# Kernel tuning notes

Hardware: AMD Instinct MI355X
Metric: run time of the kernel (lower is better)

The kernel has to match this reference:

```python
import jax, jax.numpy as jnp
import numpy as np

# ---- module config (from init_kwargs) ----
KERNEL_SIZE = 3
DIM = 3
HALF = KERNEL_SIZE // 2          # kernel offsets span [-HALF, HALF]
COORD_RANGE = 256                # voxel grid extent per spatial axis
NUM_BATCH = 4
N_VOXELS = 100_000
FEAT_DIM = 32
STRIDE = COORD_RANGE + 2 * HALF  # encoding stride so shifted coords fit


def _kernel_offsets():
    # All offsets of a KERNEL_SIZE^DIM kernel, centered (MinkowskiEngine-style).
    r = np.arange(-HALF, HALF + 1)
    grids = np.meshgrid(*([r] * DIM), indexing='ij')
    return jnp.asarray(np.stack([g.ravel() for g in grids], axis=1), dtype=jnp.int32)  # [K, DIM]


def setup_inputs() -> dict:
    key = jax.random.key(0)
    k1, k2, k3 = jax.random.split(key, 3)
    batch = jax.random.randint(k1, (1, N_VOXELS), 0, NUM_BATCH, dtype=jnp.int32)
    coords = jax.random.randint(k2, (3, N_VOXELS), 0, COORD_RANGE, dtype=jnp.int32)
    sparse_indices = jnp.concatenate([batch, coords], axis=0)  # [4, N]
    features = jax.random.normal(k3, (N_VOXELS, FEAT_DIM), dtype=jnp.float32)
    return {"sparse_indices": sparse_indices, "features": features}


def _kernel_map_and_out_key(sparse_indices):
    offsets = _kernel_offsets()                 # [K, 3]
    K = offsets.shape[0]
    b = sparse_indices[0].astype(jnp.int32)     # [N]
    coords = sparse_indices[1:].T.astype(jnp.int32)  # [N, 3]
    N = coords.shape[0]
    NK = N * K

    # neighbor coords per (voxel, offset); shift by HALF so values are >= 0
    nbr = coords[:, None, :] + offsets[None, :, :] + HALF     # [N, K, 3]
    S = STRIDE
    # unique integer hash of (batch, x, y, z); fits in int32 for these ranges
    enc = ((b[:, None] * S + nbr[..., 0]) * S + nbr[..., 1]) * S + nbr[..., 2]
    enc = enc.reshape(-1)                                     # [NK]

    # unique keys (sorted) + inverse map; pad to static size NK
    uniq, inv = jnp.unique(enc, return_inverse=True, size=NK, fill_value=-1)

    # reorder unique keys into first-seen order to match the dict-based reference
    first = jnp.full((NK,), NK, dtype=jnp.int32).at[inv].min(
        jnp.arange(NK, dtype=jnp.int32))
    order = jnp.argsort(first)                                # padding sorts last
    new_id = jnp.zeros((NK,), dtype=jnp.int32).at[order].set(
        jnp.arange(NK, dtype=jnp.int32))
    out_idx = new_id[inv]                                     # [NK] output index per entry

    # decode unique (first-seen ordered) keys back to spatial coords
    uo = uniq[order]
    valid = uo >= 0
    z = uo % S
    y = (uo // S) % S
    x = (uo // (S * S)) % S
    out_key = jnp.stack([x, y, z], axis=1) - HALF             # undo shift
    out_key = jnp.where(valid[:, None], out_key, -1)          # [NK, 3], padded rows = -1

    input_idx = jnp.repeat(jnp.arange(N, dtype=jnp.int32), K) # [NK]
    rel_pos = jnp.tile(jnp.arange(K, dtype=jnp.int32), N)     # [NK]
    kernel_map = jnp.stack([input_idx, out_idx, rel_pos], axis=1)  # [NK, 3]
    return kernel_map, out_key


def reference(sparse_indices, features):
    kernel_map, out_key = _kernel_map_and_out_key(sparse_indices)
    NK = kernel_map.shape[0]
    # canonical downstream use of the kernel map: gather inputs, scatter-sum to outputs
    out_feats = jax.ops.segment_sum(features[kernel_map[:, 0]],
                                    kernel_map[:, 1], num_segments=NK)
    return kernel_map, out_key, out_feats
```

## Files before the change

### kernel.cpp

```cpp
#include <hip/hip_runtime.h>
#include <stdint.h>

typedef unsigned long long u64;
typedef unsigned u32;
typedef float __attribute__((ext_vector_type(4))) f4raw;

#define K 27
#define S 258
#define ENCMAX (4 * S * S * S)

__global__ void k_mark(const int* __restrict__ si, int N,
                       u64* __restrict__ bits, u64* __restrict__ dupb) {
    int idx = blockIdx.x * blockDim.x + threadIdx.x;
    if (idx >= N * 9) return;
    int n = idx / 9, run = idx - n * 9;
    int ox = run / 3, oy = run - ox * 3;
    int b = si[n], x = si[N + n], y = si[2 * N + n], z = si[3 * N + n];
    unsigned enc0 = (unsigned)(((b * S + x + ox) * S + (y + oy)) * S + z);
    unsigned w = enc0 >> 6; int bit = enc0 & 63;
    u64 m1 = 7ull << bit;
    u64 old = atomicOr(&bits[w], m1);
    u64 d1 = old & m1;
    if (d1) atomicOr(&dupb[w], d1);
    if (bit > 61) {
        u64 m2 = 7ull >> (64 - bit);
        u64 old2 = atomicOr(&bits[w + 1], m2);
        u64 d2 = old2 & m2;
        if (d2) atomicOr(&dupb[w + 1], d2);
    }
}

__global__ void s1_tilesum(const u64* __restrict__ bits, int* __restrict__ tsums) {
    __shared__ int s[256];
    int tid = threadIdx.x;
    const u64* p = bits + (size_t)blockIdx.x * 4096;
    int sum = 0;
    for (int j = tid; j < 4096; j += 256) sum += __popcll(p[j]);
    s[tid] = sum; __syncthreads();
    for (int off = 128; off > 0; off >>= 1) {
        if (tid < off) s[tid] += s[tid + off];
        __syncthreads();
    }
    if (tid == 0) tsums[blockIdx.x] = s[0];
}

__global__ void s3_wprefix(const u64* __restrict__ bits, const int* __restrict__ tsums,
                           u32* __restrict__ wprefix) {
    __shared__ int s[256];
    __shared__ int tbase;
    int tid = threadIdx.x;
    int pre = 0;
    for (int j = tid; j < (int)blockIdx.x; j += 256) pre += tsums[j];
    s[tid] = pre; __syncthreads();
    for (int off = 128; off > 0; off >>= 1) {
        if (tid < off) s[tid] += s[tid + off];
        __syncthreads();
    }
    if (tid == 0) tbase = s[0];
    __syncthreads();
    size_t base = (size_t)blockIdx.x * 4096 + (size_t)tid * 16;
    int pc[16]; int tsum = 0;
#pragma unroll
    for (int j = 0; j < 16; j++) { pc[j] = __popcll(bits[base + j]); tsum += pc[j]; }
    s[tid] = tsum; __syncthreads();
    for (int off = 1; off < 256; off <<= 1) {
        int t = (tid >= off) ? s[tid - off] : 0;
        __syncthreads();
        s[tid] += t;
        __syncthreads();
    }
    int run = tbase + s[tid] - tsum;
#pragma unroll
    for (int j = 0; j < 16; j++) { wprefix[base + j] = (u32)run; run += pc[j]; }
}

__global__ void k_kid(const int* __restrict__ si, int N,
                      const u64* __restrict__ bits, const u64* __restrict__ dupb,
                      const u32* __restrict__ wprefix,
                      int* __restrict__ kid, int* __restrict__ minE) {
    int idx = blockIdx.x * blockDim.x + threadIdx.x;
    if (idx >= N * 9) return;
    int n = idx / 9, run = idx - n * 9;
    int ox = run / 3, oy = run - ox * 3;
    int b = si[n], x = si[N + n], y = si[2 * N + n], z = si[3 * N + n];
    unsigned enc0 = (unsigned)(((b * S + x + ox) * S + (y + oy)) * S + z);
    int e0 = n * K + run * 3;
#pragma unroll
    for (int oz = 0; oz < 3; ++oz) {
        unsigned enc = enc0 + oz;
        unsigned w = enc >> 6; int bit = enc & 63;
        int kd = (int)wprefix[w] + __popcll(bits[w] & ((1ull << bit) - 1));
        int multi = (int)((dupb[w] >> bit) & 1);
        kid[e0 + oz] = multi ? (int)((u32)kd | 0x80000000u) : kd;
        if (multi) atomicMin(&minE[kd], e0 + oz);
    }
}

__global__ void k_flagsum(const int* __restrict__ kid, const int* __restrict__ minE,
                          int NK, int* __restrict__ bsums) {
    __shared__ int s[256];
    int tid = threadIdx.x;
    int base = blockIdx.x * 4096 + tid * 16;
    int kv[16];
    *(int4*)(kv + 0)  = *(const int4*)(kid + base + 0);
    *(int4*)(kv + 4)  = *(const int4*)(kid + base + 4);
    *(int4*)(kv + 8)  = *(const int4*)(kid + base + 8);
    *(int4*)(kv + 12) = *(const int4*)(kid + base + 12);
    int sum = 0;
#pragma unroll
    for (int j = 0; j < 16; j++) {
        int e = base + j;
        if (e < NK) {
            int v = kv[j];
            sum += (v >= 0) ? 1 : (minE[v & 0x7FFFFFFF] == e ? 1 : 0);
        }
    }
    s[tid] = sum; __syncthreads();
    for (int off = 128; off > 0; off >>= 1) {
        if (tid < off) s[tid] += s[tid + off];
        __syncthreads();
    }
    if (tid == 0) bsums[blockIdx.x] = s[0];
}

__global__ void k_scanC(int* __restrict__ kid, const int* __restrict__ minE,
                        const int* __restrict__ bsums, const int* __restrict__ si,
                        int N, int NK, int NB,
                        float* __restrict__ out_key, int* __restrict__ rank_key,
                        float4* __restrict__ outF4) {
    __shared__ int s[256];
    __shared__ u64 s2[256];
    int tid = threadIdx.x;
    u64 acc = 0;
    for (int j = tid; j < NB; j += 256) {
        u64 b = (u64)(u32)bsums[j];
        acc += b << 32;
        if (j < (int)blockIdx.x) acc += b;
    }
    s2[tid] = acc; __syncthreads();
    for (int off = 128; off > 0; off >>= 1) {
        if (tid < off) s2[tid] += s2[tid + off];
        __syncthreads();
    }
    int blockoff = (int)(u32)(s2[0] & 0xFFFFFFFFull);
    int U = (int)(s2[0] >> 32);

    int base = blockIdx.x * 4096 + tid * 16;
    int kv[16];
    *(int4*)(kv + 0)  = *(const int4*)(kid + base + 0);
    *(int4*)(kv + 4)  = *(const int4*)(kid + base + 4);
    *(int4*)(kv + 8)  = *(const int4*)(kid + base + 8);
    *(int4*)(kv + 12) = *(const int4*)(kid + base + 12);
    int fbits = 0;
#pragma unroll
    for (int j = 0; j < 16; j++) {
        int e = base + j;
        int f = 0;
        if (e < NK) {
            int v = kv[j];
            f = (v >= 0) ? 1 : (minE[v & 0x7FFFFFFF] == e ? 1 : 0);
        }
        fbits |= f << j;
    }
    int tsum = __popc(fbits);
    s[tid] = tsum; __syncthreads();
    for (int off = 1; off < 256; off <<= 1) {
        int t = (tid >= off) ? s[tid - off] : 0;
        __syncthreads();
        s[tid] += t;
        __syncthreads();
    }
    int offset = blockoff + s[tid] - tsum;
    float4 zf = {0.f, 0.f, 0.f, 0.f};
    int run = 0;
#pragma unroll
    for (int j = 0; j < 16; j++) {
        int e = base + j;
        if ((fbits >> j) & 1) {
            int rank = offset + run;
            int n = e / K; int m = e - n * K;
            int x = si[N + n], y = si[2 * N + n], z = si[3 * N + n];
            int ox = m / 9; int rm = m - ox * 9; int oy = rm / 3; int oz = rm - oy * 3;
            out_key[(size_t)rank * 3 + 0] = (float)(x + ox - 1);
            out_key[(size_t)rank * 3 + 1] = (float)(y + oy - 1);
            out_key[(size_t)rank * 3 + 2] = (float)(z + oz - 1);
            int v = kv[j];
            if (v < 0) {
                int kd = v & 0x7FFFFFFF;
                rank_key[kd] = rank;
                kid[e] = rank | 0x40000000;
                float4* q = outF4 + (size_t)rank * 8;
#pragma unroll
                for (int q8 = 0; q8 < 8; q8++) q[q8] = zf;
            } else {
                kid[e] = rank;
            }
            run++;
        }
    }
    int rows = NK - U;
    int gs = gridDim.x * blockDim.x;
    for (int i = blockIdx.x * blockDim.x + tid; i < rows; i += gs) {
        int row = U + i;
        float4* q = outF4 + (size_t)row * 8;
#pragma unroll
        for (int q8 = 0; q8 < 8; q8++) q[q8] = zf;
        out_key[(size_t)row * 3 + 0] = -1.0f;
        out_key[(size_t)row * 3 + 1] = -1.0f;
        out_key[(size_t)row * 3 + 2] = -1.0f;
    }
}

__global__ void k_final(const int* __restrict__ ent, const int* __restrict__ rank_key,
                        const float4* __restrict__ feat4,
                        float* __restrict__ km, float* __restrict__ outF, int NK) {
    int total = NK * 8;
    int gs = gridDim.x * blockDim.x;
    for (int idx = blockIdx.x * blockDim.x + threadIdx.x; idx < total; idx += gs) {
        int e = idx >> 3, g = idx & 7;
        int v = ent[e];
        int n = e / K, m = e - n * K;
        float4 val = feat4[(size_t)n * 8 + g];
        int uid, atom;
        if (v < 0)                { uid = rank_key[v & 0x7FFFFFFF]; atom = 1; }
        else if (v & 0x40000000)  { uid = v & 0x3FFFFFFF;           atom = 1; }
        else                      { uid = v;                        atom = 0; }
        float* dst = outF + (size_t)uid * 32 + g * 4;
        if (atom) {
            atomicAdd(dst + 0, val.x);
            atomicAdd(dst + 1, val.y);
            atomicAdd(dst + 2, val.z);
            atomicAdd(dst + 3, val.w);
        } else {
            f4raw vr = {val.x, val.y, val.z, val.w};
            __builtin_nontemporal_store(vr, (f4raw*)dst);
        }
        if (g < 3)
            km[(size_t)e * 3 + g] = (g == 0) ? (float)n
                                   : ((g == 1) ? (float)uid : (float)m);
    }
}

extern "C" void kernel_launch(void* const* d_in, const int* in_sizes, int n_in,
                              void* d_out, int out_size, void* d_ws, size_t ws_size,
                              hipStream_t stream) {
    const int* si = (const int*)d_in[0];
    const float4* feat4 = (const float4*)d_in[1];
    int N = in_sizes[0] / 4;
    int NK = N * K;
    int NKp = (NK + 4095) & ~4095;
    int NB = NKp / 4096;

    int NW = (ENCMAX + 63) / 64;
    int NT = (NW + 4095) / 4096;
    int NWp = NT * 4096;

    float* km = (float*)d_out;
    float* out_key = km + (size_t)NK * 3;
    float* outF = km + (size_t)NK * 6;

    char* w = (char*)d_ws;
    char* p_bits  = w; w += ((size_t)NWp * 8 + 15) & ~(size_t)15;
    char* p_dupb  = w; w += ((size_t)NWp * 8 + 15) & ~(size_t)15;
    size_t zbytes = (size_t)(w - (char*)d_ws);
    char* p_tsums = w; w += ((size_t)(NT + 1) * 4 + 15) & ~(size_t)15;
    char* p_wpref = w; w += ((size_t)NWp * 4 + 15) & ~(size_t)15;
    char* p_minE  = w; w += ((size_t)NK * 4 + 15) & ~(size_t)15;
    char* p_kid   = w; w += ((size_t)NKp * 4 + 15) & ~(size_t)15;
    char* p_rank  = w; w += ((size_t)NK * 4 + 15) & ~(size_t)15;
    char* p_bsums = w; w += ((size_t)(NB + 1) * 4 + 15) & ~(size_t)15;

    u64* bits     = (u64*)p_bits;
    u64* dupb     = (u64*)p_dupb;
    int* tsums    = (int*)p_tsums;
    u32* wprefix  = (u32*)p_wpref;
    int* minE     = (int*)p_minE;
    int* kid      = (int*)p_kid;
    int* rank_key = (int*)p_rank;
    int* bsums    = (int*)p_bsums;

    (void)hipMemsetAsync(d_ws, 0, zbytes, stream);
    (void)hipMemsetAsync(minE, 0x7F, (size_t)NK * 4, stream);

    int nb9 = (N * 9 + 255) / 256;
    k_mark<<<nb9, 256, 0, stream>>>(si, N, bits, dupb);
    s1_tilesum<<<NT, 256, 0, stream>>>(bits, tsums);
    s3_wprefix<<<NT, 256, 0, stream>>>(bits, tsums, wprefix);
    k_kid<<<nb9, 256, 0, stream>>>(si, N, bits, dupb, wprefix, kid, minE);
    k_flagsum<<<NB, 256, 0, stream>>>(kid, minE, NK, bsums);
    k_scanC<<<NB, 256, 0, stream>>>(kid, minE, bsums, si, N, NK, NB,
                                    out_key, rank_key, (float4*)outF);
    k_final<<<2048, 256, 0, stream>>>(kid, rank_key, feat4, km, outF, NK);
}
```

Measured before the change: 607.8 us.

## Fuse hashing and scan stages into one persistent kernel with grid barriers

Merges the mark, tile-sum, word-prefix, kid, flag-sum and scan kernels into a single kernel launched with NB blocks. Hand-written atomic-counter grid barriers separate the phases. Per-entry kid values stay in registers between the kid and scan phases instead of being written and re-read, which removes several kernel launches and one global round trip. This relies on all NB blocks being resident at once (launch_bounds 256,3); if they are not, the barriers deadlock. The kid phase now works in contiguous per-thread entry chunks, so it recomputes the encoding for each entry.

```diff
diff --git a/kernel.cpp b/kernel.cpp
--- a/kernel.cpp
+++ b/kernel.cpp
@@ -9,148 +9,110 @@
 #define S 258
 #define ENCMAX (4 * S * S * S)
 
-__global__ void k_mark(const int* __restrict__ si, int N,
-                       u64* __restrict__ bits, u64* __restrict__ dupb) {
-    int idx = blockIdx.x * blockDim.x + threadIdx.x;
-    if (idx >= N * 9) return;
-    int n = idx / 9, run = idx - n * 9;
-    int ox = run / 3, oy = run - ox * 3;
-    int b = si[n], x = si[N + n], y = si[2 * N + n], z = si[3 * N + n];
-    unsigned enc0 = (unsigned)(((b * S + x + ox) * S + (y + oy)) * S + z);
-    unsigned w = enc0 >> 6; int bit = enc0 & 63;
-    u64 m1 = 7ull << bit;
-    u64 old = atomicOr(&bits[w], m1);
-    u64 d1 = old & m1;
-    if (d1) atomicOr(&dupb[w], d1);
-    if (bit > 61) {
-        u64 m2 = 7ull >> (64 - bit);
-        u64 old2 = atomicOr(&bits[w + 1], m2);
-        u64 d2 = old2 & m2;
-        if (d2) atomicOr(&dupb[w + 1], d2);
-    }
-}
-
-__global__ void s1_tilesum(const u64* __restrict__ bits, int* __restrict__ tsums) {
+__device__ __forceinline__ void gbar(int* cnt, int nblk) {
+    __syncthreads();
+    if (threadIdx.x == 0) {
+        __threadfence();
+        __hip_atomic_fetch_add(cnt, 1, __ATOMIC_RELEASE, __HIP_MEMORY_SCOPE_AGENT);
+        while (__hip_atomic_load(cnt, __ATOMIC_RELAXED, __HIP_MEMORY_SCOPE_AGENT) < nblk)
+            __builtin_amdgcn_s_sleep(2);
+        (void)__hip_atomic_load(cnt, __ATOMIC_ACQUIRE, __HIP_MEMORY_SCOPE_AGENT);
+        __threadfence();
+    }
+    __syncthreads();
+}
+
+__global__ void __launch_bounds__(256, 3)
+k_fused(const int* __restrict__ si, int N, int NK, int NT, int NB,
+        u64* __restrict__ bits, u64* __restrict__ dupb,
+        int* __restrict__ tsums, u32* __restrict__ wprefix,
+        int* __restrict__ minE, int* __restrict__ kid,
+        int* __restrict__ rank_key, float* __restrict__ out_key,
+        float4* __restrict__ outF4, int* __restrict__ barcnt) {
     __shared__ int s[256];
-    int tid = threadIdx.x;
-    const u64* p = bits + (size_t)blockIdx.x * 4096;
-    int sum = 0;
-    for (int j = tid; j < 4096; j += 256) sum += __popcll(p[j]);
-    s[tid] = sum; __syncthreads();
-    for (int off = 128; off > 0; off >>= 1) {
-        if (tid < off) s[tid] += s[tid + off];
-        __syncthreads();
-    }
-    if (tid == 0) tsums[blockIdx.x] = s[0];
-}
-
-__global__ void s3_wprefix(const u64* __restrict__ bits, const int* __restrict__ tsums,
-                           u32* __restrict__ wprefix) {
-    __shared__ int s[256];
-    __shared__ int tbase;
-    int tid = threadIdx.x;
-    int pre = 0;
-    for (int j = tid; j < (int)blockIdx.x; j += 256) pre += tsums[j];
-    s[tid] = pre; __syncthreads();
-    for (int off = 128; off > 0; off >>= 1) {
-        if (tid < off) s[tid] += s[tid + off];
-        __syncthreads();
-    }
-    if (tid == 0) tbase = s[0];
-    __syncthreads();
-    size_t base = (size_t)blockIdx.x * 4096 + (size_t)tid * 16;
+    __shared__ u64 s2[256];
+    const int tid = threadIdx.x;
+    const int b = blockIdx.x;
+    const int nblk = gridDim.x;
+    const int gs = nblk * 256;
+
+    for (int idx = b * 256 + tid; idx < N * 9; idx += gs) {
+        int n = idx / 9, run = idx - n * 9;
+        int ox = run / 3, oy = run - ox * 3;
+        int bb = si[n], x = si[N + n], y = si[2 * N + n], z = si[3 * N + n];
+        unsigned enc0 = (unsigned)(((bb * S + x + ox) * S + (y + oy)) * S + z);
+        unsigned w = enc0 >> 6; int bit = enc0 & 63;
+        u64 m1 = 7ull << bit;
+        u64 old = atomicOr(&bits[w], m1);
+        u64 d1 = old & m1;
+        if (d1) atomicOr(&dupb[w], d1);
+        if (bit > 61) {
+            u64 m2 = 7ull >> (64 - bit);
+            u64 old2 = atomicOr(&bits[w + 1], m2);
+            u64 d2 = old2 & m2;
+            if (d2) atomicOr(&dupb[w + 1], d2);
+        }
+    }
+    gbar(barcnt + 0, nblk);
+
     int pc[16]; int tsum = 0;
-#pragma unroll
-    for (int j = 0; j < 16; j++) { pc[j] = __popcll(bits[base + j]); tsum += pc[j]; }
-    s[tid] = tsum; __syncthreads();
-    for (int off = 1; off < 256; off <<= 1) {
-        int t = (tid >= off) ? s[tid - off] : 0;
-        __syncthreads();
-        s[tid] += t;
-        __syncthreads();
-    }
-    int run = tbase + s[tid] - tsum;
-#pragma unroll
-    for (int j = 0; j < 16; j++) { wprefix[base + j] = (u32)run; run += pc[j]; }
-}
-
-__global__ void k_kid(const int* __restrict__ si, int N,
-                      const u64* __restrict__ bits, const u64* __restrict__ dupb,
-                      const u32* __restrict__ wprefix,
-                      int* __restrict__ kid, int* __restrict__ minE) {
-    int idx = blockIdx.x * blockDim.x + threadIdx.x;
-    if (idx >= N * 9) return;
-    int n = idx / 9, run = idx - n * 9;
-    int ox = run / 3, oy = run - ox * 3;
-    int b = si[n], x = si[N + n], y = si[2 * N + n], z = si[3 * N + n];
-    unsigned enc0 = (unsigned)(((b * S + x + ox) * S + (y + oy)) * S + z);
-    int e0 = n * K + run * 3;
-#pragma unroll
-    for (int oz = 0; oz < 3; ++oz) {
-        unsigned enc = enc0 + oz;
-        unsigned w = enc >> 6; int bit = enc & 63;
-        int kd = (int)wprefix[w] + __popcll(bits[w] & ((1ull << bit) - 1));
-        int multi = (int)((dupb[w] >> bit) & 1);
-        kid[e0 + oz] = multi ? (int)((u32)kd | 0x80000000u) : kd;
-        if (multi) atomicMin(&minE[kd], e0 + oz);
-    }
-}
-
-__global__ void k_flagsum(const int* __restrict__ kid, const int* __restrict__ minE,
-                          int NK, int* __restrict__ bsums) {
-    __shared__ int s[256];
-    int tid = threadIdx.x;
-    int base = blockIdx.x * 4096 + tid * 16;
+    if (b < NT) {
+        size_t wb = (size_t)b * 4096 + (size_t)tid * 16;
+#pragma unroll
+        for (int j = 0; j < 16; j++) { pc[j] = __popcll(bits[wb + j]); tsum += pc[j]; }
+        s[tid] = tsum; __syncthreads();
+        for (int off = 128; off > 0; off >>= 1) {
+            if (tid < off) s[tid] += s[tid + off];
+            __syncthreads();
+        }
+        if (tid == 0) tsums[b] = s[0];
+    }
+    gbar(barcnt + 1, nblk);
+
+    if (b < NT) {
+        int pre = 0;
+        for (int j = tid; j < b; j += 256) pre += tsums[j];
+        s[tid] = pre; __syncthreads();
+        for (int off = 128; off > 0; off >>= 1) {
+            if (tid < off) s[tid] += s[tid + off];
+            __syncthreads();
+        }
+        int tbase = s[0];
+        __syncthreads();
+        s[tid] = tsum; __syncthreads();
+        for (int off = 1; off < 256; off <<= 1) {
+            int t = (tid >= off) ? s[tid - off] : 0;
+            __syncthreads();
+            s[tid] += t;
+            __syncthreads();
+        }
+        int run = tbase + s[tid] - tsum;
+        size_t wb = (size_t)b * 4096 + (size_t)tid * 16;
+#pragma unroll
+        for (int j = 0; j < 16; j++) { wprefix[wb + j] = (u32)run; run += pc[j]; }
+    }
+    gbar(barcnt + 2, nblk);
+
+    const int base = b * 4096 + tid * 16;
     int kv[16];
-    *(int4*)(kv + 0)  = *(const int4*)(kid + base + 0);
-    *(int4*)(kv + 4)  = *(const int4*)(kid + base + 4);
-    *(int4*)(kv + 8)  = *(const int4*)(kid + base + 8);
-    *(int4*)(kv + 12) = *(const int4*)(kid + base + 12);
-    int sum = 0;
 #pragma unroll
     for (int j = 0; j < 16; j++) {
         int e = base + j;
+        kv[j] = 0;
         if (e < NK) {
-            int v = kv[j];
-            sum += (v >= 0) ? 1 : (minE[v & 0x7FFFFFFF] == e ? 1 : 0);
-        }
-    }
-    s[tid] = sum; __syncthreads();
-    for (int off = 128; off > 0; off >>= 1) {
-        if (tid < off) s[tid] += s[tid + off];
-        __syncthreads();
-    }
-    if (tid == 0) bsums[blockIdx.x] = s[0];
-}
-
-__global__ void k_scanC(int* __restrict__ kid, const int* __restrict__ minE,
-                        const int* __restrict__ bsums, const int* __restrict__ si,
-                        int N, int NK, int NB,
-                        float* __restrict__ out_key, int* __restrict__ rank_key,
-                        float4* __restrict__ outF4) {
-    __shared__ int s[256];
-    __shared__ u64 s2[256];
-    int tid = threadIdx.x;
-    u64 acc = 0;
-    for (int j = tid; j < NB; j += 256) {
-        u64 b = (u64)(u32)bsums[j];
-        acc += b << 32;
-        if (j < (int)blockIdx.x) acc += b;
-    }
-    s2[tid] = acc; __syncthreads();
-    for (int off = 128; off > 0; off >>= 1) {
-        if (tid < off) s2[tid] += s2[tid + off];
-        __syncthreads();
-    }
-    int blockoff = (int)(u32)(s2[0] & 0xFFFFFFFFull);
-    int U = (int)(s2[0] >> 32);
-
-    int base = blockIdx.x * 4096 + tid * 16;
-    int kv[16];
-    *(int4*)(kv + 0)  = *(const int4*)(kid + base + 0);
-    *(int4*)(kv + 4)  = *(const int4*)(kid + base + 4);
-    *(int4*)(kv + 8)  = *(const int4*)(kid + base + 8);
-    *(int4*)(kv + 12) = *(const int4*)(kid + base + 12);
+            int n = e / K; int m = e - n * K;
+            int ox = m / 9; int rm = m - ox * 9; int oy = rm / 3; int oz = rm - oy * 3;
+            int bb = si[n], x = si[N + n], y = si[2 * N + n], z = si[3 * N + n];
+            unsigned enc = (unsigned)(((bb * S + x + ox) * S + (y + oy)) * S + (z + oz));
+            unsigned w = enc >> 6; int bit = enc & 63;
+            int kd = (int)wprefix[w] + __popcll(bits[w] & ((1ull << bit) - 1));
+            int multi = (int)((dupb[w] >> bit) & 1);
+            kv[j] = multi ? (int)((u32)kd | 0x80000000u) : kd;
+            if (multi) atomicMin(&minE[kd], e);
+        }
+    }
+    gbar(barcnt + 3, nblk);
+
     int fbits = 0;
 #pragma unroll
     for (int j = 0; j < 16; j++) {
@@ -162,45 +124,71 @@
         }
         fbits |= f << j;
     }
-    int tsum = __popc(fbits);
-    s[tid] = tsum; __syncthreads();
+    int fsum = __popc(fbits);
+    s[tid] = fsum; __syncthreads();
+    for (int off = 128; off > 0; off >>= 1) {
+        if (tid < off) s[tid] += s[tid + off];
+        __syncthreads();
+    }
+    if (tid == 0) tsums[NT + 1 + b] = s[0];
+    gbar(barcnt + 4, nblk);
+
+    const int* bsums = tsums + NT + 1;
+    u64 acc = 0;
+    for (int j = tid; j < NB; j += 256) {
+        u64 v = (u64)(u32)bsums[j];
+        acc += v << 32;
+        if (j < b) acc += v;
+    }
+    s2[tid] = acc; __syncthreads();
+    for (int off = 128; off > 0; off >>= 1) {
+        if (tid < off) s2[tid] += s2[tid + off];
+        __syncthreads();
+    }
+    int blockoff = (int)(u32)(s2[0] & 0xFFFFFFFFull);
+    int U = (int)(s2[0] >> 32);
+    __syncthreads();
+    s[tid] = fsum; __syncthreads();
     for (int off = 1; off < 256; off <<= 1) {
         int t = (tid >= off) ? s[tid - off] : 0;
         __syncthreads();
         s[tid] += t;
         __syncthreads();
     }
-    int offset = blockoff + s[tid] - tsum;
+    int offset = blockoff + s[tid] - fsum;
     float4 zf = {0.f, 0.f, 0.f, 0.f};
     int run = 0;
 #pragma unroll
     for (int j = 0; j < 16; j++) {
         int e = base + j;
-        if ((fbits >> j) & 1) {
-            int rank = offset + run;
-            int n = e / K; int m = e - n * K;
-            int x = si[N + n], y = si[2 * N + n], z = si[3 * N + n];
-            int ox = m / 9; int rm = m - ox * 9; int oy = rm / 3; int oz = rm - oy * 3;
-            out_key[(size_t)rank * 3 + 0] = (float)(x + ox - 1);
-            out_key[(size_t)rank * 3 + 1] = (float)(y + oy - 1);
-            out_key[(size_t)rank * 3 + 2] = (float)(z + oz - 1);
+        if (e < NK) {
             int v = kv[j];
-            if (v < 0) {
-                int kd = v & 0x7FFFFFFF;
-                rank_key[kd] = rank;
-                kid[e] = rank | 0x40000000;
-                float4* q = outF4 + (size_t)rank * 8;
-#pragma unroll
-                for (int q8 = 0; q8 < 8; q8++) q[q8] = zf;
+            if ((fbits >> j) & 1) {
+                int rank = offset + run;
+                int n = e / K; int m = e - n * K;
+                int x = si[N + n], y = si[2 * N + n], z = si[3 * N + n];
+                int ox = m / 9; int rm = m - ox * 9; int oy = rm / 3; int oz = rm - oy * 3;
+                out_key[(size_t)rank * 3 + 0] = (float)(x + ox - 1);
+                out_key[(size_t)rank * 3 + 1] = (float)(y + oy - 1);
+                out_key[(size_t)rank * 3 + 2] = (float)(z + oz - 1);
+                if (v < 0) {
+                    int kd = v & 0x7FFFFFFF;
+                    rank_key[kd] = rank;
+                    kid[e] = rank | 0x40000000;
+                    float4* q = outF4 + (size_t)rank * 8;
+#pragma unroll
+                    for (int q8 = 0; q8 < 8; q8++) q[q8] = zf;
+                } else {
+                    kid[e] = rank;
+                }
+                run++;
             } else {
-                kid[e] = rank;
+                kid[e] = v;
             }
-            run++;
         }
     }
     int rows = NK - U;
-    int gs = gridDim.x * blockDim.x;
-    for (int i = blockIdx.x * blockDim.x + tid; i < rows; i += gs) {
+    for (int i = b * 256 + tid; i < rows; i += gs) {
         int row = U + i;
         float4* q = outF4 + (size_t)row * 8;
 #pragma unroll
@@ -260,16 +248,17 @@
     float* outF = km + (size_t)NK * 6;
 
     char* w = (char*)d_ws;
+    char* p_bar   = w; w += 64;
     char* p_bits  = w; w += ((size_t)NWp * 8 + 15) & ~(size_t)15;
     char* p_dupb  = w; w += ((size_t)NWp * 8 + 15) & ~(size_t)15;
     size_t zbytes = (size_t)(w - (char*)d_ws);
-    char* p_tsums = w; w += ((size_t)(NT + 1) * 4 + 15) & ~(size_t)15;
+    char* p_tsums = w; w += ((size_t)(NT + 1 + NB + 1) * 4 + 15) & ~(size_t)15;
     char* p_wpref = w; w += ((size_t)NWp * 4 + 15) & ~(size_t)15;
     char* p_minE  = w; w += ((size_t)NK * 4 + 15) & ~(size_t)15;
     char* p_kid   = w; w += ((size_t)NKp * 4 + 15) & ~(size_t)15;
     char* p_rank  = w; w += ((size_t)NK * 4 + 15) & ~(size_t)15;
-    char* p_bsums = w; w += ((size_t)(NB + 1) * 4 + 15) & ~(size_t)15;
-
+
+    int* barcnt   = (int*)p_bar;
     u64* bits     = (u64*)p_bits;
     u64* dupb     = (u64*)p_dupb;
     int* tsums    = (int*)p_tsums;
@@ -277,18 +266,12 @@
     int* minE     = (int*)p_minE;
     int* kid      = (int*)p_kid;
     int* rank_key = (int*)p_rank;
-    int* bsums    = (int*)p_bsums;
 
     (void)hipMemsetAsync(d_ws, 0, zbytes, stream);
     (void)hipMemsetAsync(minE, 0x7F, (size_t)NK * 4, stream);
 
-    int nb9 = (N * 9 + 255) / 256;
-    k_mark<<<nb9, 256, 0, stream>>>(si, N, bits, dupb);
-    s1_tilesum<<<NT, 256, 0, stream>>>(bits, tsums);
-    s3_wprefix<<<NT, 256, 0, stream>>>(bits, tsums, wprefix);
-    k_kid<<<nb9, 256, 0, stream>>>(si, N, bits, dupb, wprefix, kid, minE);
-    k_flagsum<<<NB, 256, 0, stream>>>(kid, minE, NK, bsums);
-    k_scanC<<<NB, 256, 0, stream>>>(kid, minE, bsums, si, N, NK, NB,
-                                    out_key, rank_key, (float4*)outF);
+    k_fused<<<NB, 256, 0, stream>>>(si, N, NK, NT, NB, bits, dupb, tsums, wprefix,
+                                    minE, kid, rank_key, out_key, (float4*)outF,
+                                    barcnt);
     k_final<<<2048, 256, 0, stream>>>(kid, rank_key, feat4, km, outF, NK);
 }
```

Result: slower. 1.114 ms (+83.2%).

## Interleave occupancy bits, dup flag and word prefix into 16-byte records

Applied to the files above, without the earlier changes.

Packs the occupancy bitmap word, a per-word duplicate flag and the per-word prefix count into a single 16-byte record. This lets k_kid fetch everything for a lookup with one vector load instead of three scattered loads. Duplicate tracking becomes a coarse per-word flag, so more entries may take the atomic path. The bitmap scans in s1_tilesum and s3_wprefix now read with a stride of two. k_final also switches from a grid-stride loop to one thread per element.

```diff
diff --git a/kernel.cpp b/kernel.cpp
--- a/kernel.cpp
+++ b/kernel.cpp
@@ -9,8 +9,8 @@
 #define S 258
 #define ENCMAX (4 * S * S * S)
 
-__global__ void k_mark(const int* __restrict__ si, int N,
-                       u64* __restrict__ bits, u64* __restrict__ dupb) {
+
+__global__ void k_mark(const int* __restrict__ si, int N, u64* __restrict__ rec) {
     int idx = blockIdx.x * blockDim.x + threadIdx.x;
     if (idx >= N * 9) return;
     int n = idx / 9, run = idx - n * 9;
@@ -19,23 +19,21 @@
     unsigned enc0 = (unsigned)(((b * S + x + ox) * S + (y + oy)) * S + z);
     unsigned w = enc0 >> 6; int bit = enc0 & 63;
     u64 m1 = 7ull << bit;
-    u64 old = atomicOr(&bits[w], m1);
-    u64 d1 = old & m1;
-    if (d1) atomicOr(&dupb[w], d1);
+    u64 old = atomicOr(&rec[2 * (size_t)w], m1);
+    if (old & m1) atomicOr((u32*)rec + 4 * (size_t)w + 2, 1u);
     if (bit > 61) {
         u64 m2 = 7ull >> (64 - bit);
-        u64 old2 = atomicOr(&bits[w + 1], m2);
-        u64 d2 = old2 & m2;
-        if (d2) atomicOr(&dupb[w + 1], d2);
-    }
-}
-
-__global__ void s1_tilesum(const u64* __restrict__ bits, int* __restrict__ tsums) {
+        u64 old2 = atomicOr(&rec[2 * (size_t)(w + 1)], m2);
+        if (old2 & m2) atomicOr((u32*)rec + 4 * (size_t)(w + 1) + 2, 1u);
+    }
+}
+
+__global__ void s1_tilesum(const u64* __restrict__ rec, int* __restrict__ tsums) {
     __shared__ int s[256];
     int tid = threadIdx.x;
-    const u64* p = bits + (size_t)blockIdx.x * 4096;
+    const u64* p = rec + (size_t)blockIdx.x * 8192;
     int sum = 0;
-    for (int j = tid; j < 4096; j += 256) sum += __popcll(p[j]);
+    for (int j = tid; j < 4096; j += 256) sum += __popcll(p[2 * j]);
     s[tid] = sum; __syncthreads();
     for (int off = 128; off > 0; off >>= 1) {
         if (tid < off) s[tid] += s[tid + off];
@@ -44,10 +42,10 @@
     if (tid == 0) tsums[blockIdx.x] = s[0];
 }
 
-__global__ void s3_wprefix(const u64* __restrict__ bits, const int* __restrict__ tsums,
-                           u32* __restrict__ wprefix) {
+__global__ void s3_wprefix(u64* __restrict__ rec, const int* __restrict__ tsums,
+                           int NT) {
     __shared__ int s[256];
-    __shared__ int tbase;
+    __shared__ int tb;
     int tid = threadIdx.x;
     int pre = 0;
     for (int j = tid; j < (int)blockIdx.x; j += 256) pre += tsums[j];
@@ -56,12 +54,13 @@
         if (tid < off) s[tid] += s[tid + off];
         __syncthreads();
     }
-    if (tid == 0) tbase = s[0];
+    if (tid == 0) tb = s[0];
     __syncthreads();
-    size_t base = (size_t)blockIdx.x * 4096 + (size_t)tid * 16;
+    int tbase = tb;
+    size_t wb = (size_t)blockIdx.x * 4096 + (size_t)tid * 16;
     int pc[16]; int tsum = 0;
 #pragma unroll
-    for (int j = 0; j < 16; j++) { pc[j] = __popcll(bits[base + j]); tsum += pc[j]; }
+    for (int j = 0; j < 16; j++) { pc[j] = __popcll(rec[2 * (wb + j)]); tsum += pc[j]; }
     s[tid] = tsum; __syncthreads();
     for (int off = 1; off < 256; off <<= 1) {
         int t = (tid >= off) ? s[tid - off] : 0;
@@ -70,13 +69,13 @@
         __syncthreads();
     }
     int run = tbase + s[tid] - tsum;
-#pragma unroll
-    for (int j = 0; j < 16; j++) { wprefix[base + j] = (u32)run; run += pc[j]; }
+    u32* rec32 = (u32*)rec;
+#pragma unroll
+    for (int j = 0; j < 16; j++) { rec32[4 * (wb + j) + 3] = (u32)run; run += pc[j]; }
 }
 
 __global__ void k_kid(const int* __restrict__ si, int N,
-                      const u64* __restrict__ bits, const u64* __restrict__ dupb,
-                      const u32* __restrict__ wprefix,
+                      const u64* __restrict__ rec,
                       int* __restrict__ kid, int* __restrict__ minE) {
     int idx = blockIdx.x * blockDim.x + threadIdx.x;
     if (idx >= N * 9) return;
@@ -84,13 +83,25 @@
     int ox = run / 3, oy = run - ox * 3;
     int b = si[n], x = si[N + n], y = si[2 * N + n], z = si[3 * N + n];
     unsigned enc0 = (unsigned)(((b * S + x + ox) * S + (y + oy)) * S + z);
+    unsigned w = enc0 >> 6; int bit = enc0 & 63;
+    ulonglong2 r0 = *(const ulonglong2*)(rec + 2 * (size_t)w);
+    u64 bb0 = r0.x; u32 du0 = (u32)r0.y; u32 wp0 = (u32)(r0.y >> 32);
+    u64 bb1 = 0; u32 du1 = 0, wp1 = 0;
+    if (bit > 61) {
+        ulonglong2 r1 = *(const ulonglong2*)(rec + 2 * (size_t)(w + 1));
+        bb1 = r1.x; du1 = (u32)r1.y; wp1 = (u32)(r1.y >> 32);
+    }
     int e0 = n * K + run * 3;
 #pragma unroll
     for (int oz = 0; oz < 3; ++oz) {
         unsigned enc = enc0 + oz;
-        unsigned w = enc >> 6; int bit = enc & 63;
-        int kd = (int)wprefix[w] + __popcll(bits[w] & ((1ull << bit) - 1));
-        int multi = (int)((dupb[w] >> bit) & 1);
+        int bit2 = enc & 63;
+        bool hi = (enc >> 6) != w;
+        u64 bbw = hi ? bb1 : bb0;
+        u32 wp  = hi ? wp1 : wp0;
+        u32 du  = hi ? du1 : du0;
+        int kd = (int)wp + __popcll(bbw & ((1ull << bit2) - 1));
+        int multi = (du != 0);
         kid[e0 + oz] = multi ? (int)((u32)kd | 0x80000000u) : kd;
         if (multi) atomicMin(&minE[kd], e0 + oz);
     }
@@ -214,31 +225,29 @@
 __global__ void k_final(const int* __restrict__ ent, const int* __restrict__ rank_key,
                         const float4* __restrict__ feat4,
                         float* __restrict__ km, float* __restrict__ outF, int NK) {
-    int total = NK * 8;
-    int gs = gridDim.x * blockDim.x;
-    for (int idx = blockIdx.x * blockDim.x + threadIdx.x; idx < total; idx += gs) {
-        int e = idx >> 3, g = idx & 7;
-        int v = ent[e];
-        int n = e / K, m = e - n * K;
-        float4 val = feat4[(size_t)n * 8 + g];
-        int uid, atom;
-        if (v < 0)                { uid = rank_key[v & 0x7FFFFFFF]; atom = 1; }
-        else if (v & 0x40000000)  { uid = v & 0x3FFFFFFF;           atom = 1; }
-        else                      { uid = v;                        atom = 0; }
-        float* dst = outF + (size_t)uid * 32 + g * 4;
-        if (atom) {
-            atomicAdd(dst + 0, val.x);
-            atomicAdd(dst + 1, val.y);
-            atomicAdd(dst + 2, val.z);
-            atomicAdd(dst + 3, val.w);
-        } else {
-            f4raw vr = {val.x, val.y, val.z, val.w};
-            __builtin_nontemporal_store(vr, (f4raw*)dst);
-        }
-        if (g < 3)
-            km[(size_t)e * 3 + g] = (g == 0) ? (float)n
-                                   : ((g == 1) ? (float)uid : (float)m);
-    }
+    int idx = blockIdx.x * blockDim.x + threadIdx.x;
+    if (idx >= NK * 8) return;
+    int e = idx >> 3, g = idx & 7;
+    int v = ent[e];
+    int n = e / K, m = e - n * K;
+    float4 val = feat4[(size_t)n * 8 + g];
+    int uid, atom;
+    if (v < 0)                { uid = rank_key[v & 0x7FFFFFFF]; atom = 1; }
+    else if (v & 0x40000000)  { uid = v & 0x3FFFFFFF;           atom = 1; }
+    else                      { uid = v;                        atom = 0; }
+    float* dst = outF + (size_t)uid * 32 + g * 4;
+    if (atom) {
+        atomicAdd(dst + 0, val.x);
+        atomicAdd(dst + 1, val.y);
+        atomicAdd(dst + 2, val.z);
+        atomicAdd(dst + 3, val.w);
+    } else {
+        f4raw vr = {val.x, val.y, val.z, val.w};
+        __builtin_nontemporal_store(vr, (f4raw*)dst);
+    }
+    if (g < 3)
+        km[(size_t)e * 3 + g] = (g == 0) ? (float)n
+                               : ((g == 1) ? (float)uid : (float)m);
 }
 
 extern "C" void kernel_launch(void* const* d_in, const int* in_sizes, int n_in,
@@ -260,20 +269,16 @@
     float* outF = km + (size_t)NK * 6;
 
     char* w = (char*)d_ws;
-    char* p_bits  = w; w += ((size_t)NWp * 8 + 15) & ~(size_t)15;
-    char* p_dupb  = w; w += ((size_t)NWp * 8 + 15) & ~(size_t)15;
+    char* p_rec   = w; w += ((size_t)NWp * 16 + 15) & ~(size_t)15;
     size_t zbytes = (size_t)(w - (char*)d_ws);
     char* p_tsums = w; w += ((size_t)(NT + 1) * 4 + 15) & ~(size_t)15;
-    char* p_wpref = w; w += ((size_t)NWp * 4 + 15) & ~(size_t)15;
     char* p_minE  = w; w += ((size_t)NK * 4 + 15) & ~(size_t)15;
     char* p_kid   = w; w += ((size_t)NKp * 4 + 15) & ~(size_t)15;
     char* p_rank  = w; w += ((size_t)NK * 4 + 15) & ~(size_t)15;
     char* p_bsums = w; w += ((size_t)(NB + 1) * 4 + 15) & ~(size_t)15;
 
-    u64* bits     = (u64*)p_bits;
-    u64* dupb     = (u64*)p_dupb;
+    u64* rec      = (u64*)p_rec;
     int* tsums    = (int*)p_tsums;
-    u32* wprefix  = (u32*)p_wpref;
     int* minE     = (int*)p_minE;
     int* kid      = (int*)p_kid;
     int* rank_key = (int*)p_rank;
@@ -283,12 +288,13 @@
     (void)hipMemsetAsync(minE, 0x7F, (size_t)NK * 4, stream);
 
     int nb9 = (N * 9 + 255) / 256;
-    k_mark<<<nb9, 256, 0, stream>>>(si, N, bits, dupb);
-    s1_tilesum<<<NT, 256, 0, stream>>>(bits, tsums);
-    s3_wprefix<<<NT, 256, 0, stream>>>(bits, tsums, wprefix);
-    k_kid<<<nb9, 256, 0, stream>>>(si, N, bits, dupb, wprefix, kid, minE);
+    k_mark<<<nb9, 256, 0, stream>>>(si, N, rec);
+    s1_tilesum<<<NT, 256, 0, stream>>>(rec, tsums);
+    s3_wprefix<<<NT, 256, 0, stream>>>(rec, tsums, NT);
+    k_kid<<<nb9, 256, 0, stream>>>(si, N, rec, kid, minE);
     k_flagsum<<<NB, 256, 0, stream>>>(kid, minE, NK, bsums);
     k_scanC<<<NB, 256, 0, stream>>>(kid, minE, bsums, si, N, NK, NB,
                                     out_key, rank_key, (float4*)outF);
-    k_final<<<2048, 256, 0, stream>>>(kid, rank_key, feat4, km, outF, NK);
-}
+    k_final<<<(NK * 8 + 255) / 256, 256, 0, stream>>>(kid, rank_key, feat4,
+                                                      km, outF, NK);
+}
```

Result: slower. 641.2 us (+5.5%).

## Fuse tile-sum and prefix scan with grid barrier, interleave bitmap with prefix

Applied to the files above, without the earlier changes.

Merges the two scan kernels into one, joined by a software grid barrier, and keeps each block's bitmap words in registers across the barrier instead of reloading them. Each 64-bit bitmap word is then written next to its prefix count and a duplicate flag in a 16-byte record. This lets k_kid do one vector load per neighbor run instead of separate random reads of bits, wprefix and dupb. The trade-off is more memory traffic in the scan stage (full dupb read, a 16-byte-per-word table) and reliance on all blocks being co-resident for the spin barrier.

```diff
diff --git a/kernel.cpp b/kernel.cpp
--- a/kernel.cpp
+++ b/kernel.cpp
@@ -8,6 +8,19 @@
 #define K 27
 #define S 258
 #define ENCMAX (4 * S * S * S)
+
+__device__ __forceinline__ void gbar(int* cnt, int nblk) {
+    __syncthreads();
+    if (threadIdx.x == 0) {
+        __threadfence();
+        __hip_atomic_fetch_add(cnt, 1, __ATOMIC_RELEASE, __HIP_MEMORY_SCOPE_AGENT);
+        while (__hip_atomic_load(cnt, __ATOMIC_RELAXED, __HIP_MEMORY_SCOPE_AGENT) < nblk)
+            __builtin_amdgcn_s_sleep(2);
+        (void)__hip_atomic_load(cnt, __ATOMIC_ACQUIRE, __HIP_MEMORY_SCOPE_AGENT);
+        __threadfence();
+    }
+    __syncthreads();
+}
 
 __global__ void k_mark(const int* __restrict__ si, int N,
                        u64* __restrict__ bits, u64* __restrict__ dupb) {
@@ -30,38 +43,31 @@
     }
 }
 
-__global__ void s1_tilesum(const u64* __restrict__ bits, int* __restrict__ tsums) {
+__global__ void __launch_bounds__(256, 2)
+k_s13(const u64* __restrict__ bits, const u64* __restrict__ dupb,
+      int* __restrict__ tsums, u64* __restrict__ gt, int* __restrict__ barcnt) {
     __shared__ int s[256];
     int tid = threadIdx.x;
-    const u64* p = bits + (size_t)blockIdx.x * 4096;
-    int sum = 0;
-    for (int j = tid; j < 4096; j += 256) sum += __popcll(p[j]);
-    s[tid] = sum; __syncthreads();
+    int b = blockIdx.x;
+    size_t wb = (size_t)b * 4096 + (size_t)tid * 16;
+    u64 bb[16]; int pc[16]; int tsum = 0;
+#pragma unroll
+    for (int j = 0; j < 16; j++) { bb[j] = bits[wb + j]; pc[j] = __popcll(bb[j]); tsum += pc[j]; }
+    s[tid] = tsum; __syncthreads();
     for (int off = 128; off > 0; off >>= 1) {
         if (tid < off) s[tid] += s[tid + off];
         __syncthreads();
     }
-    if (tid == 0) tsums[blockIdx.x] = s[0];
-}
-
-__global__ void s3_wprefix(const u64* __restrict__ bits, const int* __restrict__ tsums,
-                           u32* __restrict__ wprefix) {
-    __shared__ int s[256];
-    __shared__ int tbase;
-    int tid = threadIdx.x;
+    if (tid == 0) tsums[b] = s[0];
+    gbar(barcnt, gridDim.x);
     int pre = 0;
-    for (int j = tid; j < (int)blockIdx.x; j += 256) pre += tsums[j];
+    for (int j = tid; j < b; j += 256) pre += tsums[j];
     s[tid] = pre; __syncthreads();
     for (int off = 128; off > 0; off >>= 1) {
         if (tid < off) s[tid] += s[tid + off];
         __syncthreads();
     }
-    if (tid == 0) tbase = s[0];
-    __syncthreads();
-    size_t base = (size_t)blockIdx.x * 4096 + (size_t)tid * 16;
-    int pc[16]; int tsum = 0;
-#pragma unroll
-    for (int j = 0; j < 16; j++) { pc[j] = __popcll(bits[base + j]); tsum += pc[j]; }
+    int tbase = s[0]; __syncthreads();
     s[tid] = tsum; __syncthreads();
     for (int off = 1; off < 256; off <<= 1) {
         int t = (tid >= off) ? s[tid - off] : 0;
@@ -71,12 +77,16 @@
     }
     int run = tbase + s[tid] - tsum;
 #pragma unroll
-    for (int j = 0; j < 16; j++) { wprefix[base + j] = (u32)run; run += pc[j]; }
+    for (int j = 0; j < 16; j++) {
+        u32 dup = (dupb[wb + j] != 0ull) ? 0x80000000u : 0u;
+        gt[2 * (wb + j)]     = bb[j];
+        gt[2 * (wb + j) + 1] = (u64)((u32)run | dup);
+        run += pc[j];
+    }
 }
 
 __global__ void k_kid(const int* __restrict__ si, int N,
-                      const u64* __restrict__ bits, const u64* __restrict__ dupb,
-                      const u32* __restrict__ wprefix,
+                      const u64* __restrict__ gt,
                       int* __restrict__ kid, int* __restrict__ minE) {
     int idx = blockIdx.x * blockDim.x + threadIdx.x;
     if (idx >= N * 9) return;
@@ -84,13 +94,24 @@
     int ox = run / 3, oy = run - ox * 3;
     int b = si[n], x = si[N + n], y = si[2 * N + n], z = si[3 * N + n];
     unsigned enc0 = (unsigned)(((b * S + x + ox) * S + (y + oy)) * S + z);
+    unsigned w = enc0 >> 6; int bit = enc0 & 63;
+    ulonglong2 r0 = *(const ulonglong2*)(gt + 2 * (size_t)w);
+    u64 bb0 = r0.x; u32 q0 = (u32)r0.y;
+    u64 bb1 = 0; u32 q1 = 0;
+    if (bit > 61) {
+        ulonglong2 r1 = *(const ulonglong2*)(gt + 2 * (size_t)(w + 1));
+        bb1 = r1.x; q1 = (u32)r1.y;
+    }
     int e0 = n * K + run * 3;
 #pragma unroll
     for (int oz = 0; oz < 3; ++oz) {
         unsigned enc = enc0 + oz;
-        unsigned w = enc >> 6; int bit = enc & 63;
-        int kd = (int)wprefix[w] + __popcll(bits[w] & ((1ull << bit) - 1));
-        int multi = (int)((dupb[w] >> bit) & 1);
+        int bit2 = enc & 63;
+        bool hi = (enc >> 6) != w;
+        u64 bbw = hi ? bb1 : bb0;
+        u32 q   = hi ? q1 : q0;
+        int kd = (int)(q & 0x7FFFFFFFu) + __popcll(bbw & ((1ull << bit2) - 1));
+        int multi = (int)(q >> 31);
         kid[e0 + oz] = multi ? (int)((u32)kd | 0x80000000u) : kd;
         if (multi) atomicMin(&minE[kd], e0 + oz);
     }
@@ -260,20 +281,22 @@
     float* outF = km + (size_t)NK * 6;
 
     char* w = (char*)d_ws;
+    char* p_bar   = w; w += 64;
     char* p_bits  = w; w += ((size_t)NWp * 8 + 15) & ~(size_t)15;
     char* p_dupb  = w; w += ((size_t)NWp * 8 + 15) & ~(size_t)15;
     size_t zbytes = (size_t)(w - (char*)d_ws);
+    char* p_gt    = w; w += ((size_t)NWp * 16 + 15) & ~(size_t)15;
     char* p_tsums = w; w += ((size_t)(NT + 1) * 4 + 15) & ~(size_t)15;
-    char* p_wpref = w; w += ((size_t)NWp * 4 + 15) & ~(size_t)15;
     char* p_minE  = w; w += ((size_t)NK * 4 + 15) & ~(size_t)15;
     char* p_kid   = w; w += ((size_t)NKp * 4 + 15) & ~(size_t)15;
     char* p_rank  = w; w += ((size_t)NK * 4 + 15) & ~(size_t)15;
     char* p_bsums = w; w += ((size_t)(NB + 1) * 4 + 15) & ~(size_t)15;
 
+    int* barcnt   = (int*)p_bar;
     u64* bits     = (u64*)p_bits;
     u64* dupb     = (u64*)p_dupb;
+    u64* gt       = (u64*)p_gt;
     int* tsums    = (int*)p_tsums;
-    u32* wprefix  = (u32*)p_wpref;
     int* minE     = (int*)p_minE;
     int* kid      = (int*)p_kid;
     int* rank_key = (int*)p_rank;
@@ -284,9 +307,8 @@
 
     int nb9 = (N * 9 + 255) / 256;
     k_mark<<<nb9, 256, 0, stream>>>(si, N, bits, dupb);
-    s1_tilesum<<<NT, 256, 0, stream>>>(bits, tsums);
-    s3_wprefix<<<NT, 256, 0, stream>>>(bits, tsums, wprefix);
-    k_kid<<<nb9, 256, 0, stream>>>(si, N, bits, dupb, wprefix, kid, minE);
+    k_s13<<<NT, 256, 0, stream>>>(bits, dupb, tsums, gt, barcnt);
+    k_kid<<<nb9, 256, 0, stream>>>(si, N, gt, kid, minE);
     k_flagsum<<<NB, 256, 0, stream>>>(kid, minE, NK, bsums);
     k_scanC<<<NB, 256, 0, stream>>>(kid, minE, bsums, si, N, NK, NB,
                                     out_key, rank_key, (float4*)outF);
```

Measured after the change: 636.1 us. 1.05x slower.
